# Performance work log

Measured on AMD Instinct MI355X. Metric: run time of the kernel, lower is better.

The kernel has to match this reference:

```python
import jax, jax.numpy as jnp
from jax import lax
import numpy as np

PATCH = 8


def setup_inputs() -> dict:
    key = jax.random.key(0)
    ks = jax.random.split(key, 6)
    B, C, H, W = 8, 128, 256, 256
    half = C // 2
    x = jax.random.normal(ks[0], (B, C, H, W), dtype=jnp.float32)
    # nn.Parameter(torch.randn(...)) -> unit normal real spectral filter
    fft_filt = jax.random.normal(ks[1], (C, PATCH, PATCH // 2 + 1), dtype=jnp.float32)
    w_in = jax.random.normal(ks[2], (C, C), dtype=jnp.float32) * 0.05
    w_before = jax.random.normal(ks[3], (half, half), dtype=jnp.float32) * 0.05
    w_dw = jax.random.normal(ks[4], (half, 1, 3, 3), dtype=jnp.float32) * 0.05
    w_out = jax.random.normal(ks[5], (C, half), dtype=jnp.float32) * 0.05
    return {"x": x, "fft_filt": fft_filt, "w_in": w_in,
            "w_before": w_before, "w_dw": w_dw, "w_out": w_out}


def reference(x, fft_filt, w_in, w_before, w_dw, w_out):
    B, C, H, W = x.shape
    p = PATCH
    pad_h = (p - H % p) % p
    pad_w = (p - W % p) % p
    xp = jnp.pad(x, ((0, 0), (0, 0), (0, pad_h), (0, pad_w))) if (pad_h or pad_w) else x
    Hp, Wp = H + pad_h, W + pad_w
    h, w = Hp // p, Wp // p

    # project_in: 1x1 conv, no bias
    y = jnp.einsum('bchw,oc->bohw', xp, w_in)

    # b c (h p1) (w p2) -> b h w c p1 p2
    yp = y.reshape(B, C, h, p, w, p).transpose(0, 2, 4, 1, 3, 5)
    yf = jnp.fft.rfft2(yp)                      # complex, last-two-axes FFT of 8x8 patches
    yf = yf * fft_filt                          # real filter broadcast over (b,h,w)
    yi = jnp.fft.irfft2(yf, s=(p, p))
    # b h w c p1 p2 -> b c (h p1) (w p2)
    y = yi.transpose(0, 3, 1, 4, 2, 5).reshape(B, C, Hp, Wp)

    # chunk + gated GELU (torch default gelu = exact erf)
    x1, x2 = jnp.split(y, 2, axis=1)
    g = jax.nn.gelu(x1, approximate=False) * x2

    # before_dwconv: 1x1 conv on half channels
    g = jnp.einsum('bchw,oc->bohw', g, w_before)
    # depthwise 3x3, padding 1
    g = lax.conv_general_dilated(g, w_dw, window_strides=(1, 1), padding='SAME',
                                 feature_group_count=C // 2,
                                 dimension_numbers=('NCHW', 'OIHW', 'NCHW'))
    # project_out: 1x1 conv half -> dim
    out = jnp.einsum('bchw,oc->bohw', g, w_out)
    out = out[:, :, :H, :W]
    return out + x
```

## Files before the change

### kernel.cpp

```cpp
#include <hip/hip_runtime.h>
#include <math.h>

#define BB 8
#define CC 128
#define HH 256
#define WW 256
#define PLANE (HH * WW)

__global__ __launch_bounds__(256) void make_k_kernel(
    const float* __restrict__ filt, float* __restrict__ kk) {
  int idx = blockIdx.x * 256 + threadIdx.x;
  if (idx >= CC * 64) return;
  int c = idx >> 6;
  int u = (idx >> 3) & 7;
  int n = idx & 7;
  const float cs8[8] = {1.f, 0.70710678118654752f, 0.f, -0.70710678118654752f,
                        -1.f, -0.70710678118654752f, 0.f, 0.70710678118654752f};
  float s = 0.f;
#pragma unroll
  for (int p = 0; p < 8; ++p) {
#pragma unroll
    for (int q = 0; q < 5; ++q) {
      float m = (q == 0 || q == 4) ? 1.f : 2.f;
      s += m * filt[(c * 8 + p) * 5 + q] * cs8[(p * u + q * n) & 7];
    }
  }
  kk[idx] = s * (1.f / 64.f);
}

__global__ __launch_bounds__(256) void fused1_kernel(
    const float* __restrict__ x, const float* __restrict__ w_in,
    const float* __restrict__ w_before, const float* __restrict__ kk,
    float* __restrict__ g2) {
  __shared__ float buf[128 * 64];
  __shared__ float gb[64 * 64];

  int bid = blockIdx.x;
  int b = bid >> 10;
  int py = (bid >> 5) & 31;
  int px = bid & 31;
  int h0 = py * 8, w0 = px * 8;
  int t = threadIdx.x;
  const float* xb = x + (size_t)b * CC * PLANE;

#pragma unroll
  for (int i = 0; i < 8; ++i) {
    int f = t + 256 * i;
    int r = f >> 1;
    int k4 = f & 1;
    int c = r >> 3, ph = r & 7;
    float4 v = *(const float4*)(xb + (size_t)c * PLANE + (size_t)(h0 + ph) * WW +
                                w0 + k4 * 4);
    *(float4*)(buf + c * 64 + ph * 8 + k4 * 4) = v;
  }
  __syncthreads();

  int ob = t >> 3;
  int pb = t & 7;

  float acc[4][8];
#pragma unroll
  for (int i = 0; i < 4; ++i)
#pragma unroll
    for (int j = 0; j < 8; ++j) acc[i][j] = 0.f;

#pragma unroll 2
  for (int c = 0; c < 128; ++c) {
    float4 lo = *(const float4*)(buf + c * 64 + pb * 8);
    float4 hi = *(const float4*)(buf + c * 64 + pb * 8 + 4);
    float xv[8] = {lo.x, lo.y, lo.z, lo.w, hi.x, hi.y, hi.z, hi.w};
#pragma unroll
    for (int i = 0; i < 4; ++i) {
      float wv = w_in[(ob * 4 + i) * 128 + c];
#pragma unroll
      for (int j = 0; j < 8; ++j) acc[i][j] += wv * xv[j];
    }
  }

  float acc2[4][8];
#pragma unroll
  for (int i = 0; i < 4; ++i)
#pragma unroll
    for (int j = 0; j < 8; ++j) acc2[i][j] = 0.f;

#pragma unroll
  for (int i = 0; i < 4; ++i) {
    int o = ob * 4 + i;
    const float* krow = kk + o * 64;
#pragma unroll
    for (int s = 0; s < 8; ++s) {
      float r8[8];
      if (s == 0) {
#pragma unroll
        for (int j = 0; j < 8; ++j) r8[j] = acc[i][j];
      } else {
        int src = (t & 56) | ((t - s) & 7);
#pragma unroll
        for (int j = 0; j < 8; ++j) r8[j] = __shfl(acc[i][j], src, 64);
      }
#pragma unroll
      for (int tt = 0; tt < 8; ++tt) {
        float kv = krow[s * 8 + tt];
#pragma unroll
        for (int j = 0; j < 8; ++j) acc2[i][j] += kv * r8[(j - tt) & 7];
      }
    }
  }
  __syncthreads();

#pragma unroll
  for (int i = 0; i < 4; ++i) {
    float* dst = buf + (ob * 4 + i) * 64 + pb * 8;
    *(float4*)dst = make_float4(acc2[i][0], acc2[i][1], acc2[i][2], acc2[i][3]);
    *(float4*)(dst + 4) =
        make_float4(acc2[i][4], acc2[i][5], acc2[i][6], acc2[i][7]);
  }
  __syncthreads();

#pragma unroll
  for (int it = 0; it < 16; ++it) {
    int f = t + it * 256;
    float a = buf[f];
    float g = buf[f + 4096];
    float ge = 0.5f * a * (1.f + erff(a * 0.70710678118654752f));
    gb[f] = ge * g;
  }
  __syncthreads();

  float acc3[2][8];
#pragma unroll
  for (int i = 0; i < 2; ++i)
#pragma unroll
    for (int j = 0; j < 8; ++j) acc3[i][j] = 0.f;

#pragma unroll 2
  for (int c = 0; c < 64; ++c) {
    float4 lo = *(const float4*)(gb + c * 64 + pb * 8);
    float4 hi = *(const float4*)(gb + c * 64 + pb * 8 + 4);
    float gv[8] = {lo.x, lo.y, lo.z, lo.w, hi.x, hi.y, hi.z, hi.w};
    float wv0 = w_before[ob * 64 + c];
    float wv1 = w_before[(ob + 32) * 64 + c];
#pragma unroll
    for (int j = 0; j < 8; ++j) {
      acc3[0][j] += wv0 * gv[j];
      acc3[1][j] += wv1 * gv[j];
    }
  }

  size_t obase = (size_t)b * 64 * PLANE + (size_t)(h0 + pb) * WW + w0;
#pragma unroll
  for (int i = 0; i < 2; ++i) {
    int o = ob + i * 32;
    float* dst = g2 + obase + (size_t)o * PLANE;
    *(float4*)dst = make_float4(acc3[i][0], acc3[i][1], acc3[i][2], acc3[i][3]);
    *(float4*)(dst + 4) =
        make_float4(acc3[i][4], acc3[i][5], acc3[i][6], acc3[i][7]);
  }
}

__global__ __launch_bounds__(256) void dwconv_kernel(
    const float* __restrict__ g2, const float* __restrict__ w_dw,
    float* __restrict__ dout) {
  int wseg = blockIdx.x;
  int hseg = blockIdx.y;
  int bc = blockIdx.z;
  int c = bc & 63;
  const float* src = g2 + (size_t)bc * PLANE;
  float* dst = dout + (size_t)bc * PLANE;
  __shared__ float tile[10][66];
  int w0 = wseg * 64, h0 = hseg * 8;
  int t = threadIdx.x;
  for (int f = t; f < 660; f += 256) {
    int r = f / 66, cl = f - r * 66;
    int hh = h0 + r - 1, ww = w0 + cl - 1;
    float v = 0.f;
    if (hh >= 0 && hh < HH && ww >= 0 && ww < WW) v = src[hh * WW + ww];
    tile[r][cl] = v;
  }
  float k9[9];
#pragma unroll
  for (int i = 0; i < 9; ++i) k9[i] = w_dw[c * 9 + i];
  __syncthreads();
#pragma unroll
  for (int rep = 0; rep < 2; ++rep) {
    int r = rep * 4 + (t >> 6);
    int cl = t & 63;
    float s = 0.f;
#pragma unroll
    for (int i = 0; i < 3; ++i)
#pragma unroll
      for (int j = 0; j < 3; ++j) s += k9[i * 3 + j] * tile[r + i][cl + j];
    dst[(size_t)(h0 + r) * WW + w0 + cl] = s;
  }
}

__global__ __launch_bounds__(256) void mixout_kernel(
    const float* __restrict__ d, const float* __restrict__ w_out,
    const float* __restrict__ x, float* __restrict__ out) {
  int bid = blockIdx.x;
  int wseg = bid & 3;
  int hh = (bid >> 2) & 255;
  int b = bid >> 10;
  __shared__ float ds[64 * 64];
  int t = threadIdx.x;
  const float* dbase = d + (size_t)b * 64 * PLANE + (size_t)hh * WW + wseg * 64;
#pragma unroll
  for (int i = 0; i < 4; ++i) {
    int f = t + 256 * i;
    int c = f >> 4, k4 = f & 15;
    *(float4*)(ds + c * 64 + k4 * 4) =
        *(const float4*)(dbase + (size_t)c * PLANE + k4 * 4);
  }
  __syncthreads();
  int o2 = t >> 3, pb = t & 7;
  float acc[4][8];
#pragma unroll
  for (int i = 0; i < 4; ++i)
#pragma unroll
    for (int j = 0; j < 8; ++j) acc[i][j] = 0.f;

#pragma unroll 2
  for (int c = 0; c < 64; ++c) {
    float4 lo = *(const float4*)(ds + c * 64 + pb * 8);
    float4 hi = *(const float4*)(ds + c * 64 + pb * 8 + 4);
    float gv[8] = {lo.x, lo.y, lo.z, lo.w, hi.x, hi.y, hi.z, hi.w};
#pragma unroll
    for (int i = 0; i < 4; ++i) {
      float wv = w_out[(o2 + i * 32) * 64 + c];
#pragma unroll
      for (int j = 0; j < 8; ++j) acc[i][j] += wv * gv[j];
    }
  }

  size_t base =
      (size_t)b * CC * PLANE + (size_t)hh * WW + (size_t)wseg * 64 + pb * 8;
#pragma unroll
  for (int i = 0; i < 4; ++i) {
    int o = o2 + i * 32;
    const float* xp = x + base + (size_t)o * PLANE;
    float* op = out + base + (size_t)o * PLANE;
    float4 xlo = *(const float4*)xp;
    float4 xhi = *(const float4*)(xp + 4);
    float4 r0 = make_float4(acc[i][0] + xlo.x, acc[i][1] + xlo.y,
                            acc[i][2] + xlo.z, acc[i][3] + xlo.w);
    float4 r1 = make_float4(acc[i][4] + xhi.x, acc[i][5] + xhi.y,
                            acc[i][6] + xhi.z, acc[i][7] + xhi.w);
    *(float4*)op = r0;
    *(float4*)(op + 4) = r1;
  }
}

extern "C" void kernel_launch(void* const* d_in, const int* in_sizes, int n_in,
                              void* d_out, int out_size, void* d_ws,
                              size_t ws_size, hipStream_t stream) {
  const float* x = (const float*)d_in[0];
  const float* fft_filt = (const float*)d_in[1];
  const float* w_in = (const float*)d_in[2];
  const float* w_before = (const float*)d_in[3];
  const float* w_dw = (const float*)d_in[4];
  const float* w_out = (const float*)d_in[5];
  float* out = (float*)d_out;

  char* ws = (char*)d_ws;
  float* kk = (float*)ws;
  float* g2 = (float*)(ws + (1 << 16));
  float* dbuf = g2 + (size_t)BB * 64 * PLANE;

  hipLaunchKernelGGL(make_k_kernel, dim3(32), dim3(256), 0, stream, fft_filt,
                     kk);
  hipLaunchKernelGGL(fused1_kernel, dim3(8192), dim3(256), 0, stream, x, w_in,
                     w_before, kk, g2);
  hipLaunchKernelGGL(dwconv_kernel, dim3(4, 32, 512), dim3(256), 0, stream, g2,
                     w_dw, dbuf);
  hipLaunchKernelGGL(mixout_kernel, dim3(8192), dim3(256), 0, stream, dbuf,
                     w_out, x, out);
}
```

Baseline: 1.334 ms.

## Pre-transpose weights for vector loads, shrink LDS, enlarge dwconv tiles, remap mixout

A prep kernel now transposes w_in, w_before, w_out and the spatial filter kernel so each thread can fetch several output-channel weights with one vector load instead of scalar strided loads. In fused1 the circular shift is now applied one step at a time to all four accumulator rows, and the separate gb shared buffer is dropped to cut LDS use and raise occupancy. The depthwise conv tile grows from 8 to 32 rows per block to reduce halo reloads. mixout switches to one pixel per thread with 32 output channels as wave-uniform weights, giving coalesced scalar stores in place of float4 stores, at the cost of more registers.

```diff
diff --git a/kernel.cpp b/kernel.cpp
--- a/kernel.cpp
+++ b/kernel.cpp
@@ -7,33 +7,48 @@
 #define WW 256
 #define PLANE (HH * WW)
 
-__global__ __launch_bounds__(256) void make_k_kernel(
-    const float* __restrict__ filt, float* __restrict__ kk) {
+__global__ __launch_bounds__(256) void prep_kernel(
+    const float* __restrict__ filt, const float* __restrict__ w_in,
+    const float* __restrict__ w_before, const float* __restrict__ w_out,
+    float* __restrict__ kkt, float* __restrict__ w_in_t,
+    float* __restrict__ w_before_t, float* __restrict__ w_out_t) {
   int idx = blockIdx.x * 256 + threadIdx.x;
-  if (idx >= CC * 64) return;
-  int c = idx >> 6;
-  int u = (idx >> 3) & 7;
-  int n = idx & 7;
-  const float cs8[8] = {1.f, 0.70710678118654752f, 0.f, -0.70710678118654752f,
-                        -1.f, -0.70710678118654752f, 0.f, 0.70710678118654752f};
-  float s = 0.f;
-#pragma unroll
-  for (int p = 0; p < 8; ++p) {
-#pragma unroll
-    for (int q = 0; q < 5; ++q) {
-      float m = (q == 0 || q == 4) ? 1.f : 2.f;
-      s += m * filt[(c * 8 + p) * 5 + q] * cs8[(p * u + q * n) & 7];
-    }
-  }
-  kk[idx] = s * (1.f / 64.f);
+  if (idx < 8192) {
+    int c = idx >> 6;
+    int un = idx & 63;
+    int u = un >> 3, n = un & 7;
+    const float cs8[8] = {1.f,  0.70710678118654752f,  0.f, -0.70710678118654752f,
+                          -1.f, -0.70710678118654752f, 0.f, 0.70710678118654752f};
+    float s = 0.f;
+#pragma unroll
+    for (int p = 0; p < 8; ++p) {
+#pragma unroll
+      for (int q = 0; q < 5; ++q) {
+        float m = (q == 0 || q == 4) ? 1.f : 2.f;
+        s += m * filt[(c * 8 + p) * 5 + q] * cs8[(p * u + q * n) & 7];
+      }
+    }
+    kkt[un * 128 + c] = s * (1.f / 64.f);
+  } else if (idx < 24576) {
+    int j = idx - 8192;
+    int o = j >> 7, c = j & 127;
+    w_in_t[c * 128 + o] = w_in[o * 128 + c];
+  } else if (idx < 28672) {
+    int j = idx - 24576;
+    int o = j >> 6, c = j & 63;
+    w_before_t[c * 64 + o] = w_before[o * 64 + c];
+  } else if (idx < 36864) {
+    int j = idx - 28672;
+    int o = j >> 6, c = j & 63;
+    w_out_t[c * 128 + o] = w_out[o * 64 + c];
+  }
 }
 
 __global__ __launch_bounds__(256) void fused1_kernel(
-    const float* __restrict__ x, const float* __restrict__ w_in,
-    const float* __restrict__ w_before, const float* __restrict__ kk,
+    const float* __restrict__ x, const float* __restrict__ w_in_t,
+    const float* __restrict__ w_before_t, const float* __restrict__ kkt,
     float* __restrict__ g2) {
   __shared__ float buf[128 * 64];
-  __shared__ float gb[64 * 64];
 
   int bid = blockIdx.x;
   int b = bid >> 10;
@@ -49,8 +64,8 @@
     int r = f >> 1;
     int k4 = f & 1;
     int c = r >> 3, ph = r & 7;
-    float4 v = *(const float4*)(xb + (size_t)c * PLANE + (size_t)(h0 + ph) * WW +
-                                w0 + k4 * 4);
+    float4 v = *(const float4*)(xb + (size_t)c * PLANE +
+                                (size_t)(h0 + ph) * WW + w0 + k4 * 4);
     *(float4*)(buf + c * 64 + ph * 8 + k4 * 4) = v;
   }
   __syncthreads();
@@ -64,17 +79,19 @@
 #pragma unroll
     for (int j = 0; j < 8; ++j) acc[i][j] = 0.f;
 
-#pragma unroll 2
+  const float* wp = w_in_t + ob * 4;
+  const float* bp = buf + pb * 8;
+#pragma unroll 4
   for (int c = 0; c < 128; ++c) {
-    float4 lo = *(const float4*)(buf + c * 64 + pb * 8);
-    float4 hi = *(const float4*)(buf + c * 64 + pb * 8 + 4);
+    float4 lo = *(const float4*)(bp + c * 64);
+    float4 hi = *(const float4*)(bp + c * 64 + 4);
+    float4 wv = *(const float4*)(wp + c * 128);
     float xv[8] = {lo.x, lo.y, lo.z, lo.w, hi.x, hi.y, hi.z, hi.w};
-#pragma unroll
-    for (int i = 0; i < 4; ++i) {
-      float wv = w_in[(ob * 4 + i) * 128 + c];
-#pragma unroll
-      for (int j = 0; j < 8; ++j) acc[i][j] += wv * xv[j];
-    }
+    float wa[4] = {wv.x, wv.y, wv.z, wv.w};
+#pragma unroll
+    for (int i = 0; i < 4; ++i)
+#pragma unroll
+      for (int j = 0; j < 8; ++j) acc[i][j] += wa[i] * xv[j];
   }
 
   float acc2[4][8];
@@ -83,27 +100,31 @@
 #pragma unroll
     for (int j = 0; j < 8; ++j) acc2[i][j] = 0.f;
 
-#pragma unroll
-  for (int i = 0; i < 4; ++i) {
-    int o = ob * 4 + i;
-    const float* krow = kk + o * 64;
-#pragma unroll
-    for (int s = 0; s < 8; ++s) {
-      float r8[8];
-      if (s == 0) {
-#pragma unroll
-        for (int j = 0; j < 8; ++j) r8[j] = acc[i][j];
-      } else {
-        int src = (t & 56) | ((t - s) & 7);
-#pragma unroll
-        for (int j = 0; j < 8; ++j) r8[j] = __shfl(acc[i][j], src, 64);
-      }
-#pragma unroll
-      for (int tt = 0; tt < 8; ++tt) {
-        float kv = krow[s * 8 + tt];
-#pragma unroll
-        for (int j = 0; j < 8; ++j) acc2[i][j] += kv * r8[(j - tt) & 7];
-      }
+  float r8[4][8];
+#pragma unroll
+  for (int i = 0; i < 4; ++i)
+#pragma unroll
+    for (int j = 0; j < 8; ++j) r8[i][j] = acc[i][j];
+
+  const float* kb = kkt + ob * 4;
+  int srcm1 = (t & 56) | ((t - 1) & 7);
+#pragma unroll
+  for (int s = 0; s < 8; ++s) {
+    if (s > 0) {
+#pragma unroll
+      for (int i = 0; i < 4; ++i)
+#pragma unroll
+        for (int j = 0; j < 8; ++j) r8[i][j] = __shfl(r8[i][j], srcm1, 64);
+    }
+#pragma unroll
+    for (int tt = 0; tt < 8; ++tt) {
+      float4 kv = *(const float4*)(kb + (s * 8 + tt) * 128);
+      float ka[4] = {kv.x, kv.y, kv.z, kv.w};
+#pragma unroll
+      for (int i = 0; i < 4; ++i)
+#pragma unroll
+        for (int j = 0; j < 8; ++j)
+          acc2[i][j] += ka[i] * r8[i][(j - tt) & 7];
     }
   }
   __syncthreads();
@@ -123,7 +144,7 @@
     float a = buf[f];
     float g = buf[f + 4096];
     float ge = 0.5f * a * (1.f + erff(a * 0.70710678118654752f));
-    gb[f] = ge * g;
+    buf[f] = ge * g;
   }
   __syncthreads();
 
@@ -133,24 +154,24 @@
 #pragma unroll
     for (int j = 0; j < 8; ++j) acc3[i][j] = 0.f;
 
-#pragma unroll 2
+  const float* wbp = w_before_t + ob * 2;
+#pragma unroll 4
   for (int c = 0; c < 64; ++c) {
-    float4 lo = *(const float4*)(gb + c * 64 + pb * 8);
-    float4 hi = *(const float4*)(gb + c * 64 + pb * 8 + 4);
+    float4 lo = *(const float4*)(bp + c * 64);
+    float4 hi = *(const float4*)(bp + c * 64 + 4);
+    float2 wv = *(const float2*)(wbp + c * 64);
     float gv[8] = {lo.x, lo.y, lo.z, lo.w, hi.x, hi.y, hi.z, hi.w};
-    float wv0 = w_before[ob * 64 + c];
-    float wv1 = w_before[(ob + 32) * 64 + c];
 #pragma unroll
     for (int j = 0; j < 8; ++j) {
-      acc3[0][j] += wv0 * gv[j];
-      acc3[1][j] += wv1 * gv[j];
+      acc3[0][j] += wv.x * gv[j];
+      acc3[1][j] += wv.y * gv[j];
     }
   }
 
   size_t obase = (size_t)b * 64 * PLANE + (size_t)(h0 + pb) * WW + w0;
 #pragma unroll
   for (int i = 0; i < 2; ++i) {
-    int o = ob + i * 32;
+    int o = ob * 2 + i;
     float* dst = g2 + obase + (size_t)o * PLANE;
     *(float4*)dst = make_float4(acc3[i][0], acc3[i][1], acc3[i][2], acc3[i][3]);
     *(float4*)(dst + 4) =
@@ -167,10 +188,10 @@
   int c = bc & 63;
   const float* src = g2 + (size_t)bc * PLANE;
   float* dst = dout + (size_t)bc * PLANE;
-  __shared__ float tile[10][66];
-  int w0 = wseg * 64, h0 = hseg * 8;
+  __shared__ float tile[34][66];
+  int w0 = wseg * 64, h0 = hseg * 32;
   int t = threadIdx.x;
-  for (int f = t; f < 660; f += 256) {
+  for (int f = t; f < 34 * 66; f += 256) {
     int r = f / 66, cl = f - r * 66;
     int hh = h0 + r - 1, ww = w0 + cl - 1;
     float v = 0.f;
@@ -181,10 +202,10 @@
 #pragma unroll
   for (int i = 0; i < 9; ++i) k9[i] = w_dw[c * 9 + i];
   __syncthreads();
-#pragma unroll
-  for (int rep = 0; rep < 2; ++rep) {
+  int cl = t & 63;
+#pragma unroll
+  for (int rep = 0; rep < 8; ++rep) {
     int r = rep * 4 + (t >> 6);
-    int cl = t & 63;
     float s = 0.f;
 #pragma unroll
     for (int i = 0; i < 3; ++i)
@@ -195,7 +216,7 @@
 }
 
 __global__ __launch_bounds__(256) void mixout_kernel(
-    const float* __restrict__ d, const float* __restrict__ w_out,
+    const float* __restrict__ d, const float* __restrict__ w_out_t,
     const float* __restrict__ x, float* __restrict__ out) {
   int bid = blockIdx.x;
   int wseg = bid & 3;
@@ -212,41 +233,27 @@
         *(const float4*)(dbase + (size_t)c * PLANE + k4 * 4);
   }
   __syncthreads();
-  int o2 = t >> 3, pb = t & 7;
-  float acc[4][8];
-#pragma unroll
-  for (int i = 0; i < 4; ++i)
-#pragma unroll
-    for (int j = 0; j < 8; ++j) acc[i][j] = 0.f;
-
+
+  int og = __builtin_amdgcn_readfirstlane(t >> 6);
+  int pix = t & 63;
+  float acc[32];
+#pragma unroll
+  for (int i = 0; i < 32; ++i) acc[i] = 0.f;
+
+  const float* wt = w_out_t + og * 32;
 #pragma unroll 2
   for (int c = 0; c < 64; ++c) {
-    float4 lo = *(const float4*)(ds + c * 64 + pb * 8);
-    float4 hi = *(const float4*)(ds + c * 64 + pb * 8 + 4);
-    float gv[8] = {lo.x, lo.y, lo.z, lo.w, hi.x, hi.y, hi.z, hi.w};
-#pragma unroll
-    for (int i = 0; i < 4; ++i) {
-      float wv = w_out[(o2 + i * 32) * 64 + c];
-#pragma unroll
-      for (int j = 0; j < 8; ++j) acc[i][j] += wv * gv[j];
-    }
-  }
-
-  size_t base =
-      (size_t)b * CC * PLANE + (size_t)hh * WW + (size_t)wseg * 64 + pb * 8;
-#pragma unroll
-  for (int i = 0; i < 4; ++i) {
-    int o = o2 + i * 32;
-    const float* xp = x + base + (size_t)o * PLANE;
-    float* op = out + base + (size_t)o * PLANE;
-    float4 xlo = *(const float4*)xp;
-    float4 xhi = *(const float4*)(xp + 4);
-    float4 r0 = make_float4(acc[i][0] + xlo.x, acc[i][1] + xlo.y,
-                            acc[i][2] + xlo.z, acc[i][3] + xlo.w);
-    float4 r1 = make_float4(acc[i][4] + xhi.x, acc[i][5] + xhi.y,
-                            acc[i][6] + xhi.z, acc[i][7] + xhi.w);
-    *(float4*)op = r0;
-    *(float4*)(op + 4) = r1;
+    float xv = ds[c * 64 + pix];
+#pragma unroll
+    for (int i = 0; i < 32; ++i) acc[i] += wt[c * 128 + i] * xv;
+  }
+
+  size_t pbase =
+      (size_t)b * CC * PLANE + (size_t)hh * WW + (size_t)wseg * 64 + pix;
+#pragma unroll
+  for (int i = 0; i < 32; ++i) {
+    int o = og * 32 + i;
+    out[pbase + (size_t)o * PLANE] = acc[i] + x[pbase + (size_t)o * PLANE];
   }
 }
 
@@ -262,16 +269,19 @@
   float* out = (float*)d_out;
 
   char* ws = (char*)d_ws;
-  float* kk = (float*)ws;
-  float* g2 = (float*)(ws + (1 << 16));
+  float* kkt = (float*)ws;
+  float* w_in_t = kkt + 8192;
+  float* w_before_t = w_in_t + 16384;
+  float* w_out_t = w_before_t + 4096;
+  float* g2 = (float*)(ws + (1 << 20));
   float* dbuf = g2 + (size_t)BB * 64 * PLANE;
 
-  hipLaunchKernelGGL(make_k_kernel, dim3(32), dim3(256), 0, stream, fft_filt,
-                     kk);
-  hipLaunchKernelGGL(fused1_kernel, dim3(8192), dim3(256), 0, stream, x, w_in,
-                     w_before, kk, g2);
-  hipLaunchKernelGGL(dwconv_kernel, dim3(4, 32, 512), dim3(256), 0, stream, g2,
+  hipLaunchKernelGGL(prep_kernel, dim3(144), dim3(256), 0, stream, fft_filt,
+                     w_in, w_before, w_out, kkt, w_in_t, w_before_t, w_out_t);
+  hipLaunchKernelGGL(fused1_kernel, dim3(8192), dim3(256), 0, stream, x,
+                     w_in_t, w_before_t, kkt, g2);
+  hipLaunchKernelGGL(dwconv_kernel, dim3(4, 8, 512), dim3(256), 0, stream, g2,
                      w_dw, dbuf);
   hipLaunchKernelGGL(mixout_kernel, dim3(8192), dim3(256), 0, stream, dbuf,
-                     w_out, x, out);
-}
+                     w_out_t, x, out);
+}
```

Result: faster. 1.217 ms (-8.7%).
